# Optimization experiments

Hardware: AMD Instinct MI355X
Metric: run time of the kernel (lower is better)

## Reference

```python
import jax, jax.numpy as jnp
import numpy as np

N_COM = 100  # number of communities


def _gat(x, src, dst, ew, W, a_s, a_d):
    # Weighted multi-head GAT layer. x: [N,F], src/dst: [E], ew: [E]
    N = x.shape[0]
    H, dh = a_s.shape
    h = (x @ W).reshape(N, H, dh)              # [N,H,dh]
    hs, hd = h[src], h[dst]                     # [E,H,dh]
    e = jax.nn.leaky_relu((hs * a_s).sum(-1) + (hd * a_d).sum(-1), 0.2)  # [E,H]
    m = jax.ops.segment_max(e, dst, num_segments=N)  # [N,H] stable softmax max
    m = jnp.where(jnp.isfinite(m), m, 0.0)
    ex = jnp.exp(e - m[dst]) * ew[:, None]      # edge-weighted attention numerator
    den = jax.ops.segment_sum(ex, dst, num_segments=N)          # [N,H]
    num = jax.ops.segment_sum(ex[:, :, None] * hs, dst, num_segments=N)  # [N,H,dh]
    out = num / (den[:, :, None] + 1e-16)
    return jax.nn.elu(out.reshape(N, H * dh))


def _meso(x, part, D):
    # WeiPool_noW: degree-weighted mean pooling per community, scattered back to nodes
    num = jax.ops.segment_sum(D[:, None] * x, part, num_segments=N_COM)  # [C,d]
    den = jax.ops.segment_sum(D, part, num_segments=N_COM)               # [C]
    mean = num / (den[:, None] + 1e-16)
    return mean[part]                                                     # [N,d]


def _lstm_cell(h, c, x, Wx, Wh, b):
    z = x @ Wx + h @ Wh + b
    i, f, g, o = jnp.split(z, 4, axis=-1)
    c = jax.nn.sigmoid(f) * c + jax.nn.sigmoid(i) * jnp.tanh(g)
    h = jax.nn.sigmoid(o) * jnp.tanh(c)
    return h, c


def setup_inputs() -> dict:
    key = jax.random.key(0)
    ks = jax.random.split(key, 20)
    T, N, E, F = 8, 10000, 320000, 128
    H = 4
    d1, d2 = 128, 64            # micro_dims[1], micro_dims[2]
    d_rnn = 128                 # RNN_dims[1]; RNN input = 2*d2 = 128
    d_dec = 64                  # decoder_dims[1]
    s = 0.05
    inp = {
        'feat': jax.random.normal(ks[0], (T, N, F), jnp.float32),
        'edge_weight': jax.random.uniform(ks[1], (T, E), jnp.float32),
        'D': jax.random.uniform(ks[2], (T, N), jnp.float32),
        'W1': jax.random.normal(ks[3], (F, d1), jnp.float32) * s,
        'a_src1': jax.random.normal(ks[4], (H, d1 // H), jnp.float32) * s,
        'a_dst1': jax.random.normal(ks[5], (H, d1 // H), jnp.float32) * s,
        'W2': jax.random.normal(ks[6], (d1, d2), jnp.float32) * s,
        'a_src2': jax.random.normal(ks[7], (H, d2 // H), jnp.float32) * s,
        'a_dst2': jax.random.normal(ks[8], (H, d2 // H), jnp.float32) * s,
        'Wx': jax.random.normal(ks[9], (2 * d2, 4 * d_rnn), jnp.float32) * s,
        'Wh': jax.random.normal(ks[10], (d_rnn, 4 * d_rnn), jnp.float32) * s,
        'b_lstm': jnp.zeros((4 * d_rnn,), jnp.float32),
        'emb_W': jax.random.normal(ks[11], (d_rnn, d_dec), jnp.float32) * s,
        'emb_b': jnp.zeros((d_dec,), jnp.float32),
        'scal_W': jax.random.normal(ks[12], (d_rnn, d_dec), jnp.float32) * s,
        'scal_b': jnp.zeros((d_dec,), jnp.float32),
        'edge_index': jax.random.randint(ks[13], (T, 2, E), 0, N, jnp.int64),
        'partition': jax.random.randint(ks[14], (T, N), 0, N_COM, jnp.int64),
    }
    return inp


def reference(feat, edge_weight, D, W1, a_src1, a_dst1, W2, a_src2, a_dst2,
              Wx, Wh, b_lstm, emb_W, emb_b, scal_W, scal_b,
              edge_index, partition):
    T, N, _ = feat.shape
    src, dst = edge_index[:, 0], edge_index[:, 1]          # [T,E]
    gat = jax.vmap(_gat, in_axes=(0, 0, 0, 0, None, None, None))
    g1 = gat(feat, src, dst, edge_weight, W1, a_src1, a_dst1)   # [T,N,d1]
    g2 = gat(g1, src, dst, edge_weight, W2, a_src2, a_dst2)     # [T,N,d2]
    meso = jax.vmap(_meso)(g2, partition, D)                    # [T,N,d2]
    agg = jnp.concatenate([g2, meso], axis=-1)                  # [T,N,2*d2]

    d_h = Wh.shape[0]
    h0 = jnp.zeros((N, d_h), feat.dtype)

    def step(carry, x):
        h, c = carry
        h, c = _lstm_cell(h, c, x, Wx, Wh, b_lstm)
        return (h, c), h

    _, hs = jax.lax.scan(step, (h0, h0), agg)                   # [T,N,d_h]
    h_last = hs[-1]

    emb = jnp.tanh(h_last @ emb_W + emb_b)                      # decoder emb path
    emb = emb / jnp.linalg.norm(emb, axis=0, keepdims=True)     # F.normalize dim=0
    scal = jax.nn.sigmoid(h_last @ scal_W + scal_b)             # decoder scal path
    S = scal @ scal.T                                            # [N,N]
    G = emb @ emb.T
    sq = jnp.diag(G)
    dist = -(sq[:, None] + sq[None, :] - 2.0 * G)                # -||e_i - e_j||^2
    adj_est = 1.0 + jnp.tanh(dist * S)
    return adj_est
```

## Files before the change

### kernel.cpp

```cpp
#include <hip/hip_runtime.h>
#include <cstddef>
#include <cstdint>

#define T_   8
#define N_   10000
#define E_   320000
#define F_   128
#define D1_  128
#define D2_  64
#define DR_  128
#define NC_  100
#define TN_  (T_*N_)
#define TE_  (T_*E_)
#define NPAD_ 10112

typedef __attribute__((ext_vector_type(8))) short bf16x8;
typedef __attribute__((ext_vector_type(8))) ushort u16x8;
typedef __attribute__((ext_vector_type(4))) float f32x4;

__device__ __forceinline__ float bf2f(ushort u) {
    return __uint_as_float(((unsigned int)u) << 16);
}
__device__ __forceinline__ ushort f2bf(float f) {
    unsigned int u = __float_as_uint(f);
    unsigned int r = (u + 0x7FFFu + ((u >> 16) & 1u)) >> 16;
    return (ushort)r;
}
__device__ __forceinline__ float fast_tanh(float x) {
    float t = __expf(2.f * x);
    return 1.f - 2.f / (t + 1.f);
}
__device__ __forceinline__ float fast_sigmoid(float x) {
    return 1.f / (1.f + __expf(-x));
}

__global__ __launch_bounds__(256) void conv_feat(const float* __restrict__ src,
                                                 ushort* __restrict__ dst, int n8)
{
    int idx = blockIdx.x * 256 + threadIdx.x;
    if (idx >= n8) return;
    const float4* s = (const float4*)src + (size_t)idx * 2;
    float4 x = s[0], y = s[1];
    u16x8 o;
    o[0]=f2bf(x.x); o[1]=f2bf(x.y); o[2]=f2bf(x.z); o[3]=f2bf(x.w);
    o[4]=f2bf(y.x); o[5]=f2bf(y.y); o[6]=f2bf(y.z); o[7]=f2bf(y.w);
    *((u16x8*)dst + idx) = o;
}

__global__ __launch_bounds__(256) void conv_weights(
    const float* __restrict__ W1, const float* __restrict__ W2,
    const float* __restrict__ Wx, const float* __restrict__ Wh,
    const float* __restrict__ eW, const float* __restrict__ sW,
    ushort* __restrict__ W1T, ushort* __restrict__ W2T,
    ushort* __restrict__ WxT, ushort* __restrict__ WhT,
    ushort* __restrict__ eWT, ushort* __restrict__ sWT)
{
    int idx = blockIdx.x * 256 + threadIdx.x;
    if (idx < 16384)       { int n=idx>>7,   k=idx&127;            W1T[idx]=f2bf(W1[k*128+n]); }
    else if (idx < 24576)  { int l=idx-16384;  int n=l>>7,k=l&127; W2T[l]=f2bf(W2[k*64+n]); }
    else if (idx < 90112)  { int l=idx-24576;  int n=l>>7,k=l&127; WxT[l]=f2bf(Wx[k*512+n]); }
    else if (idx < 155648) { int l=idx-90112;  int n=l>>7,k=l&127; WhT[l]=f2bf(Wh[k*512+n]); }
    else if (idx < 163840) { int l=idx-155648; int n=l>>7,k=l&127; eWT[l]=f2bf(eW[k*64+n]); }
    else if (idx < 172032) { int l=idx-163840; int n=l>>7,k=l&127; sWT[l]=f2bf(sW[k*64+n]); }
}

__global__ __launch_bounds__(256) void gemm_bf16(
    const ushort* __restrict__ A, const ushort* __restrict__ BT,
    float* __restrict__ Cf, ushort* __restrict__ Cb,
    const float* __restrict__ bias, const float* __restrict__ addsrc,
    int M, int K, int Nc, int act)
{
    int w = threadIdx.x >> 6, lane = threadIdx.x & 63;
    int quad = lane >> 4, l16 = lane & 15;
    int m0 = blockIdx.y * 128 + w * 32;
    int n0 = blockIdx.x * 64;
    f32x4 zf = {0.f, 0.f, 0.f, 0.f};
    f32x4 acc[2][4];
    #pragma unroll
    for (int rt = 0; rt < 2; ++rt)
        #pragma unroll
        for (int ct = 0; ct < 4; ++ct) acc[rt][ct] = zf;

    for (int k0 = 0; k0 < K; k0 += 32) {
        int kk = k0 + quad * 8;
        bf16x8 a0 = *(const bf16x8*)(A + (size_t)(m0 + l16) * K + kk);
        bf16x8 a1 = *(const bf16x8*)(A + (size_t)(m0 + 16 + l16) * K + kk);
        bf16x8 b[4];
        #pragma unroll
        for (int ct = 0; ct < 4; ++ct)
            b[ct] = *(const bf16x8*)(BT + (size_t)(n0 + ct * 16 + l16) * K + kk);
        #pragma unroll
        for (int ct = 0; ct < 4; ++ct) {
            acc[0][ct] = __builtin_amdgcn_mfma_f32_16x16x32_bf16(a0, b[ct], acc[0][ct], 0, 0, 0);
            acc[1][ct] = __builtin_amdgcn_mfma_f32_16x16x32_bf16(a1, b[ct], acc[1][ct], 0, 0, 0);
        }
    }

    #pragma unroll
    for (int rt = 0; rt < 2; ++rt) {
        int ibase = m0 + rt * 16 + quad * 4;
        #pragma unroll
        for (int r = 0; r < 4; ++r) {
            int i = ibase + r;
            if (i >= M) continue;
            #pragma unroll
            for (int ct = 0; ct < 4; ++ct) {
                int j = n0 + ct * 16 + l16;
                float v = acc[rt][ct][r];
                if (bias)   v += bias[j];
                if (addsrc) v += addsrc[(size_t)i * Nc + j];
                if (act == 1)      v = fast_tanh(v);
                else if (act == 2) v = fast_sigmoid(v);
                if (Cf) Cf[(size_t)i * Nc + j] = v;
                if (Cb) Cb[(size_t)i * Nc + j] = f2bf(v);
            }
        }
    }
}

__global__ __launch_bounds__(256) void att_vec128(
    const ushort* __restrict__ h, const float* __restrict__ a_src,
    const float* __restrict__ a_dst, float* __restrict__ as_out,
    float* __restrict__ ad_out, int rows)
{
    int wid  = (blockIdx.x * 256 + threadIdx.x) >> 6;
    int lane = threadIdx.x & 63;
    if (wid >= rows) return;
    const ushort* hr = h + (size_t)wid * 128;
    float v0 = bf2f(hr[lane]), v1 = bf2f(hr[64 + lane]);
    float pa0 = v0 * a_src[lane], pa1 = v1 * a_src[64 + lane];
    float pd0 = v0 * a_dst[lane], pd1 = v1 * a_dst[64 + lane];
    #pragma unroll
    for (int m = 1; m <= 16; m <<= 1) {
        pa0 += __shfl_xor(pa0, m); pa1 += __shfl_xor(pa1, m);
        pd0 += __shfl_xor(pd0, m); pd1 += __shfl_xor(pd1, m);
    }
    if ((lane & 31) == 0) {
        int g = lane >> 5;
        as_out[wid * 4 + g] = pa0; as_out[wid * 4 + 2 + g] = pa1;
        ad_out[wid * 4 + g] = pd0; ad_out[wid * 4 + 2 + g] = pd1;
    }
}

__global__ __launch_bounds__(256) void att_vec64(
    const ushort* __restrict__ h, const float* __restrict__ a_src,
    const float* __restrict__ a_dst, float* __restrict__ as_out,
    float* __restrict__ ad_out, int rows)
{
    int wid  = (blockIdx.x * 256 + threadIdx.x) >> 6;
    int lane = threadIdx.x & 63;
    if (wid >= rows) return;
    float v = bf2f(h[(size_t)wid * 64 + lane]);
    float pa = v * a_src[lane], pd = v * a_dst[lane];
    #pragma unroll
    for (int m = 1; m <= 8; m <<= 1) { pa += __shfl_xor(pa, m); pd += __shfl_xor(pd, m); }
    if ((lane & 15) == 0) {
        int g = lane >> 4;
        as_out[wid * 4 + g] = pa; ad_out[wid * 4 + g] = pd;
    }
}

__global__ void count_edges(const int* __restrict__ eidx, int* __restrict__ counts)
{
    int idx = blockIdx.x * 256 + threadIdx.x;
    if (idx >= TE_) return;
    int t = idx / E_, e = idx - t * E_;
    int d = eidx[(size_t)t * 2 * E_ + E_ + e];
    atomicAdd(&counts[t * N_ + d], 1);
}

__global__ __launch_bounds__(1024) void scan_per_t(
    const int* __restrict__ counts, int* __restrict__ rowptr, int* __restrict__ cursor)
{
    const int CH = 10;
    int t = blockIdx.x, i = threadIdx.x;
    int base0 = t * N_;
    int cnt[CH];
    int s = 0;
    int g0 = i * CH;
    #pragma unroll
    for (int q = 0; q < CH; ++q) {
        int g = g0 + q;
        cnt[q] = (g < N_) ? counts[base0 + g] : 0;
        s += cnt[q];
    }
    __shared__ int buf[1024];
    buf[i] = s;
    __syncthreads();
    for (int off = 1; off < 1024; off <<= 1) {
        int v = (i >= off) ? buf[i - off] : 0;
        __syncthreads();
        buf[i] += v;
        __syncthreads();
    }
    int run = t * E_ + buf[i] - s;
    #pragma unroll
    for (int q = 0; q < CH; ++q) {
        int g = g0 + q;
        if (g < N_) {
            rowptr[base0 + g] = run;
            cursor[base0 + g] = run;
            run += cnt[q];
        }
    }
    if (t == T_ - 1 && i == 1023) rowptr[T_ * N_] = TE_;
}

__global__ void fill_csr(const int* __restrict__ eidx, const float* __restrict__ ew,
                         int* __restrict__ cursor, int* __restrict__ src_csr,
                         float* __restrict__ ew_csr)
{
    int idx = blockIdx.x * 256 + threadIdx.x;
    if (idx >= TE_) return;
    int t = idx / E_, e = idx - t * E_;
    int s = eidx[(size_t)t * 2 * E_ + e];
    int d = eidx[(size_t)t * 2 * E_ + E_ + e];
    float w = ew[(size_t)t * E_ + e];
    int pos = atomicAdd(&cursor[t * N_ + d], 1);
    src_csr[pos] = t * N_ + s;
    ew_csr[pos] = w;
}

__global__ __launch_bounds__(256) void gat_node_128(
    const ushort* __restrict__ h, const float* __restrict__ as,
    const float* __restrict__ ad, const int* __restrict__ rowptr,
    const int* __restrict__ src_csr, const float* __restrict__ ew_csr,
    ushort* __restrict__ outp, int rows)
{
    int wid  = (blockIdx.x * 256 + threadIdx.x) >> 6;
    int lane = threadIdx.x & 63;
    if (wid >= rows) return;
    int start = rowptr[wid], end = rowptr[wid + 1];
    int h0 = lane >> 5, h1 = 2 + h0;
    float ad0 = ad[wid * 4 + h0], ad1 = ad[wid * 4 + h1];
    float acc0 = 0.f, acc1 = 0.f, den0 = 0.f, den1 = 0.f;
    for (int p = start; p < end; ++p) {
        int s = src_csr[p];
        float w = ew_csr[p];
        float e0 = as[s * 4 + h0] + ad0; e0 = e0 > 0.f ? e0 : 0.2f * e0;
        float e1 = as[s * 4 + h1] + ad1; e1 = e1 > 0.f ? e1 : 0.2f * e1;
        float x0 = __expf(e0) * w;
        float x1 = __expf(e1) * w;
        den0 += x0; den1 += x1;
        const ushort* hs = h + (size_t)s * 128;
        acc0 += x0 * bf2f(hs[lane]);
        acc1 += x1 * bf2f(hs[64 + lane]);
    }
    float o0 = acc0 / (den0 + 1e-16f);
    float o1 = acc1 / (den1 + 1e-16f);
    o0 = o0 > 0.f ? o0 : (__expf(o0) - 1.f);
    o1 = o1 > 0.f ? o1 : (__expf(o1) - 1.f);
    outp[(size_t)wid * 128 + lane]      = f2bf(o0);
    outp[(size_t)wid * 128 + 64 + lane] = f2bf(o1);
}

__global__ __launch_bounds__(256) void gat_node_64(
    const ushort* __restrict__ h, const float* __restrict__ as,
    const float* __restrict__ ad, const int* __restrict__ rowptr,
    const int* __restrict__ src_csr, const float* __restrict__ ew_csr,
    ushort* __restrict__ outp, int rows)
{
    int wid  = (blockIdx.x * 256 + threadIdx.x) >> 6;
    int lane = threadIdx.x & 63;
    if (wid >= rows) return;
    int start = rowptr[wid], end = rowptr[wid + 1];
    int hh = lane >> 4;
    float adv = ad[wid * 4 + hh];
    float acc = 0.f, den = 0.f;
    for (int p = start; p < end; ++p) {
        int s = src_csr[p];
        float w = ew_csr[p];
        float e = as[s * 4 + hh] + adv; e = e > 0.f ? e : 0.2f * e;
        float x = __expf(e) * w;
        den += x;
        acc += x * bf2f(h[(size_t)s * 64 + lane]);
    }
    float o = acc / (den + 1e-16f);
    o = o > 0.f ? o : (__expf(o) - 1.f);
    outp[(size_t)wid * 64 + lane] = f2bf(o);
}

__global__ __launch_bounds__(256) void meso_acc(
    const ushort* __restrict__ g2, const int* __restrict__ part,
    const float* __restrict__ Dw, float* __restrict__ msum, float* __restrict__ mden)
{
    int wid  = (blockIdx.x * 256 + threadIdx.x) >> 6;
    int lane = threadIdx.x & 63;
    if (wid >= TN_) return;
    int t = wid / N_;
    int p = part[wid];
    float dv = Dw[wid];
    atomicAdd(&msum[((size_t)(t * NC_ + p) << 6) + lane], dv * bf2f(g2[(size_t)wid * 64 + lane]));
    if (lane == 0) atomicAdd(&mden[t * NC_ + p], dv);
}

__global__ void agg_assemble(
    const ushort* __restrict__ g2, const int* __restrict__ part,
    const float* __restrict__ msum, const float* __restrict__ mden,
    ushort* __restrict__ agg)
{
    int idx = blockIdx.x * 256 + threadIdx.x;
    int row = idx >> 7, d = idx & 127;
    ushort v;
    if (d < 64) {
        v = g2[(size_t)row * 64 + d];
    } else {
        int t = row / N_;
        int p = part[row];
        v = f2bf(msum[((size_t)(t * NC_ + p) << 6) + (d - 64)] / (mden[t * NC_ + p] + 1e-16f));
    }
    agg[idx] = v;
}

__global__ void lstm_cell(const float* __restrict__ z, float* __restrict__ c,
                          ushort* __restrict__ hb)
{
    int idx = blockIdx.x * 256 + threadIdx.x;
    int n = idx >> 7, j = idx & 127;
    const float* zr = z + (size_t)n * 512;
    float zi = zr[j], zf = zr[128 + j], zg = zr[256 + j], zo = zr[384 + j];
    float si = fast_sigmoid(zi);
    float sf = fast_sigmoid(zf);
    float so = fast_sigmoid(zo);
    float cn = sf * c[idx] + si * fast_tanh(zg);
    c[idx] = cn;
    hb[(size_t)n * 128 + j] = f2bf(so * fast_tanh(cn));
}

__global__ __launch_bounds__(256) void col_sumsq(const float* __restrict__ emb,
                                                 float* __restrict__ colss)
{
    int tid = threadIdx.x;
    int col = tid & 63, rq = tid >> 6;
    float s = 0.f;
    for (int r = blockIdx.x * 4 + rq; r < N_; r += 40 * 4) {
        float v = emb[(size_t)r * 64 + col];
        s += v * v;
    }
    __shared__ float red[256];
    red[tid] = s;
    __syncthreads();
    if (tid < 64)
        atomicAdd(&colss[tid], red[tid] + red[tid + 64] + red[tid + 128] + red[tid + 192]);
}

__global__ __launch_bounds__(256) void norm_rows(const float* __restrict__ emb,
                                                 const float* __restrict__ colss,
                                                 ushort* __restrict__ embb,
                                                 float* __restrict__ sq, int rows)
{
    int wid  = (blockIdx.x * 256 + threadIdx.x) >> 6;
    int lane = threadIdx.x & 63;
    if (wid >= rows) return;
    float nv = emb[(size_t)wid * 64 + lane] / sqrtf(colss[lane]);
    ushort ub = f2bf(nv);
    embb[(size_t)wid * 64 + lane] = ub;
    float nq = bf2f(ub);
    float q = nq * nq;
    #pragma unroll
    for (int m = 1; m <= 32; m <<= 1) q += __shfl_xor(q, m);
    if (lane == 0) sq[wid] = q;
}

#define FTJ_   5
#define FCOLS_ (FTJ_*128)

__global__ __launch_bounds__(256) void final_adj_mfma(
    const ushort* __restrict__ embb, const ushort* __restrict__ scalb,
    const float* __restrict__ sq, float* __restrict__ outp)
{
    __shared__ float cur[128][132];
    __shared__ float edg[2][64][16];

    int w = threadIdx.x >> 6, lane = threadIdx.x & 63;
    int quad = lane >> 4, l16 = lane & 15;
    int bi = blockIdx.y * 128;
    int Wb = blockIdx.x * FCOLS_;
    int wi = bi + (w >> 1) * 64;

    float sqi[4];
    #pragma unroll
    for (int rt = 0; rt < 4; ++rt) sqi[rt] = sq[wi + rt * 16 + l16];

    int tLast = (N_ - 1 - Wb) / 128;
    if (tLast > FTJ_ - 1) tLast = FTJ_ - 1;

    for (int t = 0; t <= tLast; ++t) {
        int Wt = Wb + t * 128;
        int wj = Wt + (w & 1) * 64;

        f32x4 zf = {0.f, 0.f, 0.f, 0.f};
        f32x4 accG[4][4], accS[4][4];
        #pragma unroll
        for (int rt = 0; rt < 4; ++rt)
            #pragma unroll
            for (int ct = 0; ct < 4; ++ct) { accG[rt][ct] = zf; accS[rt][ct] = zf; }

        #pragma unroll
        for (int ks = 0; ks < 2; ++ks) {
            int k0 = ks * 32 + quad * 8;
            bf16x8 ae[4], af[4], be[4], bs[4];
            #pragma unroll
            for (int q = 0; q < 4; ++q) {
                int ri = wi + q * 16 + l16;
                int rj = wj + q * 16 + l16;
                ae[q] = *(const bf16x8*)(embb  + (size_t)ri * 64 + k0);
                af[q] = *(const bf16x8*)(scalb + (size_t)ri * 64 + k0);
                be[q] = *(const bf16x8*)(embb  + (size_t)rj * 64 + k0);
                bs[q] = *(const bf16x8*)(scalb + (size_t)rj * 64 + k0);
            }
            #pragma unroll
            for (int rt = 0; rt < 4; ++rt)
                #pragma unroll
                for (int ct = 0; ct < 4; ++ct) {
                    accG[rt][ct] = __builtin_amdgcn_mfma_f32_16x16x32_bf16(be[ct], ae[rt], accG[rt][ct], 0, 0, 0);
                    accS[rt][ct] = __builtin_amdgcn_mfma_f32_16x16x32_bf16(bs[ct], af[rt], accS[rt][ct], 0, 0, 0);
                }
        }

        __syncthreads();

        #pragma unroll
        for (int rt = 0; rt < 4; ++rt) {
            int li = (w >> 1) * 64 + rt * 16 + l16;
            float si = sqi[rt];
            #pragma unroll
            for (int ct = 0; ct < 4; ++ct) {
                int lj = (w & 1) * 64 + ct * 16 + quad * 4;
                const float4 sj = *(const float4*)(sq + Wt + lj);
                float sjr[4] = { sj.x, sj.y, sj.z, sj.w };
                f32x4 v;
                #pragma unroll
                for (int r = 0; r < 4; ++r) {
                    float G = accG[rt][ct][r], S = accS[rt][ct][r];
                    float dist = 2.f * G - si - sjr[r];
                    float e = __expf(2.f * dist * S);
                    v[r] = 2.f - 2.f / (e + 1.f);
                }
                *(f32x4*)&cur[li][lj] = v;
                if ((w & 1) && ct == 3 && (li & 1))
                    *(f32x4*)&edg[t & 1][li >> 1][quad * 4] = v;
            }
        }

        __syncthreads();

        int lane5 = lane & 31;
        #pragma unroll
        for (int pass = 0; pass < 16; ++pass) {
            int r = pass * 8 + (lane >> 5) * 4 + w;
            int i = bi + r;
            if (i < N_) {
                if (!(r & 1)) {
                    int gcol = Wt + lane5 * 4;
                    if (gcol < N_)
                        __builtin_nontemporal_store(*(const f32x4*)&cur[r][lane5 * 4],
                            (f32x4*)(outp + (size_t)i * N_ + gcol));
                } else {
                    int gcol = Wt - 16 + lane5 * 4;
                    if ((t > 0 || lane5 >= 4) && gcol >= 0 && gcol < N_) {
                        f32x4 v;
                        if (lane5 < 4) v = *(const f32x4*)&edg[(t & 1) ^ 1][r >> 1][lane5 * 4];
                        else           v = *(const f32x4*)&cur[r][lane5 * 4 - 16];
                        __builtin_nontemporal_store(v,
                            (f32x4*)(outp + (size_t)i * N_ + gcol));
                    }
                }
            }
        }
    }

    {
        int tid = threadIdx.x;
        int r = ((tid >> 2) << 1) | 1;
        int k = (tid & 3) * 4;
        int i = bi + r;
        int gcol = Wb + tLast * 128 + 112 + k;
        if (i < N_ && gcol < N_) {
            f32x4 v = *(const f32x4*)&cur[r][112 + k];
            __builtin_nontemporal_store(v, (f32x4*)(outp + (size_t)i * N_ + gcol));
        }
    }
}

extern "C" void kernel_launch(void* const* d_in, const int* in_sizes, int n_in,
                              void* d_out, int out_size, void* d_ws, size_t ws_size,
                              hipStream_t stream)
{
    (void)in_sizes; (void)n_in; (void)out_size; (void)ws_size;
    const float* feat    = (const float*)d_in[0];
    const float* eweight = (const float*)d_in[1];
    const float* Dw      = (const float*)d_in[2];
    const float* W1      = (const float*)d_in[3];
    const float* a_src1  = (const float*)d_in[4];
    const float* a_dst1  = (const float*)d_in[5];
    const float* W2      = (const float*)d_in[6];
    const float* a_src2  = (const float*)d_in[7];
    const float* a_dst2  = (const float*)d_in[8];
    const float* Wx      = (const float*)d_in[9];
    const float* Wh      = (const float*)d_in[10];
    const float* b_lstm  = (const float*)d_in[11];
    const float* emb_W   = (const float*)d_in[12];
    const float* emb_b   = (const float*)d_in[13];
    const float* scal_W  = (const float*)d_in[14];
    const float* scal_b  = (const float*)d_in[15];
    const int*   eidx    = (const int*)d_in[16];
    const int*   part    = (const int*)d_in[17];

    float* out = (float*)d_out;
    ushort* h1b   = (ushort*)(out + 0);
    ushort* g1b   = (ushort*)(out + 5120000);
    ushort* h2b   = (ushort*)(out + 10240000);
    ushort* g2b   = (ushort*)(out + 12800000);
    float* as1    = out + 15360000;
    float* ad1    = out + 15680000;
    float* as2    = out + 16000000;
    float* ad2    = out + 16320000;
    int*   rowptr = (int*)(out + 16640000);
    int*   cursor = (int*)(out + 16720064);
    int*   counts = (int*)(out + 16800064);
    int*   src_csr= (int*)(out + 16880064);
    float* ew_csr = out + 19440064;
    float* msum   = out + 22000064;
    float* mden   = out + 22051264;
    ushort* aggb  = (ushort*)(out + 22052064);
    float* ZX     = out + 27172064;
    float* zbuf   = out + 68132064;
    float* cstate = out + 73252064;
    ushort* hbf   = (ushort*)(out + 74532064);
    ushort* featb = (ushort*)(out + 75179232);
    ushort* W1T   = (ushort*)(out + 80299232);
    ushort* W2T   = (ushort*)(out + 80307424);
    ushort* WxT   = (ushort*)(out + 80311520);
    ushort* WhT   = (ushort*)(out + 80344288);
    ushort* eWT   = (ushort*)(out + 80377056);
    ushort* sWT   = (ushort*)(out + 80381152);
    float* embf   = out + 80385248;
    float* colss  = out + 81025248;

    ushort* embb  = (ushort*)d_ws;
    ushort* scalb = embb + (size_t)NPAD_ * 64;
    float*  sq    = (float*)(scalb + (size_t)NPAD_ * 64);

    hipMemsetAsync(counts, 0, TN_ * sizeof(int), stream);
    hipMemsetAsync(msum, 0, (T_ * NC_ * 64 + T_ * NC_) * sizeof(float), stream);
    hipMemsetAsync(cstate, 0, (size_t)N_ * DR_ * sizeof(float), stream);
    hipMemsetAsync(hbf, 0, (size_t)NPAD_ * DR_ * sizeof(ushort), stream);
    hipMemsetAsync(colss, 0, 64 * sizeof(float), stream);

    conv_feat<<<5000, 256, 0, stream>>>(feat, featb, TN_ * F_ / 8);
    conv_weights<<<672, 256, 0, stream>>>(W1, W2, Wx, Wh, emb_W, scal_W,
                                          W1T, W2T, WxT, WhT, eWT, sWT);

    gemm_bf16<<<dim3(2, 625), 256, 0, stream>>>(featb, W1T, nullptr, h1b, nullptr, nullptr, TN_, 128, 128, 0);
    att_vec128<<<TN_/4, 256, 0, stream>>>(h1b, a_src1, a_dst1, as1, ad1, TN_);
    count_edges<<<(TE_+255)/256, 256, 0, stream>>>(eidx, counts);
    scan_per_t<<<T_, 1024, 0, stream>>>(counts, rowptr, cursor);
    fill_csr<<<(TE_+255)/256, 256, 0, stream>>>(eidx, eweight, cursor, src_csr, ew_csr);
    gat_node_128<<<TN_/4, 256, 0, stream>>>(h1b, as1, ad1, rowptr, src_csr, ew_csr, g1b, TN_);

    gemm_bf16<<<dim3(1, 625), 256, 0, stream>>>(g1b, W2T, nullptr, h2b, nullptr, nullptr, TN_, 128, 64, 0);
    att_vec64<<<TN_/4, 256, 0, stream>>>(h2b, a_src2, a_dst2, as2, ad2, TN_);
    gat_node_64<<<TN_/4, 256, 0, stream>>>(h2b, as2, ad2, rowptr, src_csr, ew_csr, g2b, TN_);

    meso_acc<<<TN_/4, 256, 0, stream>>>(g2b, part, Dw, msum, mden);
    agg_assemble<<<TN_*128/256, 256, 0, stream>>>(g2b, part, msum, mden, aggb);

    gemm_bf16<<<dim3(8, 625), 256, 0, stream>>>(aggb, WxT, ZX, nullptr, b_lstm, nullptr, TN_, 128, 512, 0);
    for (int t = 0; t < T_; ++t) {
        gemm_bf16<<<dim3(8, 79), 256, 0, stream>>>(hbf, WhT, zbuf, nullptr, nullptr,
                                                   ZX + (size_t)t * N_ * 512, N_, 128, 512, 0);
        lstm_cell<<<N_*DR_/256, 256, 0, stream>>>(zbuf, cstate, hbf);
    }

    gemm_bf16<<<dim3(1, 79), 256, 0, stream>>>(hbf, eWT, embf, nullptr, emb_b, nullptr, N_, 128, 64, 1);
    gemm_bf16<<<dim3(1, 79), 256, 0, stream>>>(hbf, sWT, nullptr, scalb, scal_b, nullptr, N_, 128, 64, 2);
    col_sumsq<<<40, 256, 0, stream>>>(embf, colss);
    norm_rows<<<(N_+3)/4, 256, 0, stream>>>(embf, colss, embb, sq, N_);

    final_adj_mfma<<<dim3(16, 79), 256, 0, stream>>>(embb, scalb, sq, out);
}
```

Baseline: 1.870 ms.

## Fuse LSTM recurrent GEMM with cell update and unroll GAT edge loops

Replaces the per-timestep recurrent gemm plus separate lstm_cell kernel with one MFMA kernel. It computes h@Wh for a 32-row tile, adds the precomputed input projection, stages the gates in shared memory and applies the cell update in place. This removes the fp32 zbuf write and read-back and one launch per step. Separately, both GAT aggregation kernels now process four edges per iteration and load the four per-head attention scores with a single float4. This exposes more independent gathers. Costs are a large shared-memory tile and higher register pressure.

```diff
diff --git a/kernel.cpp b/kernel.cpp
--- a/kernel.cpp
+++ b/kernel.cpp
@@ -231,21 +231,46 @@
     int lane = threadIdx.x & 63;
     if (wid >= rows) return;
     int start = rowptr[wid], end = rowptr[wid + 1];
-    int h0 = lane >> 5, h1 = 2 + h0;
-    float ad0 = ad[wid * 4 + h0], ad1 = ad[wid * 4 + h1];
+    int h0 = lane >> 5;
+    float ad0 = ad[wid * 4 + h0], ad1 = ad[wid * 4 + 2 + h0];
     float acc0 = 0.f, acc1 = 0.f, den0 = 0.f, den1 = 0.f;
-    for (int p = start; p < end; ++p) {
+
+    int p = start;
+    for (; p + 4 <= end; p += 4) {
+        int s0 = src_csr[p+0], s1 = src_csr[p+1], s2 = src_csr[p+2], s3 = src_csr[p+3];
+        float w0 = ew_csr[p+0], w1 = ew_csr[p+1], w2 = ew_csr[p+2], w3 = ew_csr[p+3];
+        float4 A0 = *(const float4*)(as + (size_t)s0 * 4);
+        float4 A1 = *(const float4*)(as + (size_t)s1 * 4);
+        float4 A2 = *(const float4*)(as + (size_t)s2 * 4);
+        float4 A3 = *(const float4*)(as + (size_t)s3 * 4);
+        const ushort* q0 = h + (size_t)s0 * 128;
+        const ushort* q1 = h + (size_t)s1 * 128;
+        const ushort* q2 = h + (size_t)s2 * 128;
+        const ushort* q3 = h + (size_t)s3 * 128;
+        float hx0 = bf2f(q0[lane]), hy0 = bf2f(q0[64 + lane]);
+        float hx1 = bf2f(q1[lane]), hy1 = bf2f(q1[64 + lane]);
+        float hx2 = bf2f(q2[lane]), hy2 = bf2f(q2[64 + lane]);
+        float hx3 = bf2f(q3[lane]), hy3 = bf2f(q3[64 + lane]);
+        #define GSTEP(AA, ww, hx, hy) { \
+            float e0 = (h0 ? AA.y : AA.x) + ad0; e0 = e0 > 0.f ? e0 : 0.2f * e0; \
+            float e1 = (h0 ? AA.w : AA.z) + ad1; e1 = e1 > 0.f ? e1 : 0.2f * e1; \
+            float x0 = __expf(e0) * ww, x1 = __expf(e1) * ww; \
+            den0 += x0; den1 += x1; acc0 += x0 * hx; acc1 += x1 * hy; }
+        GSTEP(A0, w0, hx0, hy0)
+        GSTEP(A1, w1, hx1, hy1)
+        GSTEP(A2, w2, hx2, hy2)
+        GSTEP(A3, w3, hx3, hy3)
+    }
+    for (; p < end; ++p) {
         int s = src_csr[p];
         float w = ew_csr[p];
-        float e0 = as[s * 4 + h0] + ad0; e0 = e0 > 0.f ? e0 : 0.2f * e0;
-        float e1 = as[s * 4 + h1] + ad1; e1 = e1 > 0.f ? e1 : 0.2f * e1;
-        float x0 = __expf(e0) * w;
-        float x1 = __expf(e1) * w;
-        den0 += x0; den1 += x1;
-        const ushort* hs = h + (size_t)s * 128;
-        acc0 += x0 * bf2f(hs[lane]);
-        acc1 += x1 * bf2f(hs[64 + lane]);
-    }
+        float4 A = *(const float4*)(as + (size_t)s * 4);
+        const ushort* q = h + (size_t)s * 128;
+        float hx = bf2f(q[lane]), hy = bf2f(q[64 + lane]);
+        GSTEP(A, w, hx, hy)
+    }
+    #undef GSTEP
+
     float o0 = acc0 / (den0 + 1e-16f);
     float o1 = acc1 / (den1 + 1e-16f);
     o0 = o0 > 0.f ? o0 : (__expf(o0) - 1.f);
@@ -267,14 +292,38 @@
     int hh = lane >> 4;
     float adv = ad[wid * 4 + hh];
     float acc = 0.f, den = 0.f;
-    for (int p = start; p < end; ++p) {
+
+    int p = start;
+    for (; p + 4 <= end; p += 4) {
+        int s0 = src_csr[p+0], s1 = src_csr[p+1], s2 = src_csr[p+2], s3 = src_csr[p+3];
+        float w0 = ew_csr[p+0], w1 = ew_csr[p+1], w2 = ew_csr[p+2], w3 = ew_csr[p+3];
+        float4 A0 = *(const float4*)(as + (size_t)s0 * 4);
+        float4 A1 = *(const float4*)(as + (size_t)s1 * 4);
+        float4 A2 = *(const float4*)(as + (size_t)s2 * 4);
+        float4 A3 = *(const float4*)(as + (size_t)s3 * 4);
+        float hv0 = bf2f(h[(size_t)s0 * 64 + lane]);
+        float hv1 = bf2f(h[(size_t)s1 * 64 + lane]);
+        float hv2 = bf2f(h[(size_t)s2 * 64 + lane]);
+        float hv3 = bf2f(h[(size_t)s3 * 64 + lane]);
+        #define GSTEP64(AA, ww, hv) { \
+            float e = (hh & 2 ? (hh & 1 ? AA.w : AA.z) : (hh & 1 ? AA.y : AA.x)) + adv; \
+            e = e > 0.f ? e : 0.2f * e; \
+            float x = __expf(e) * ww; \
+            den += x; acc += x * hv; }
+        GSTEP64(A0, w0, hv0)
+        GSTEP64(A1, w1, hv1)
+        GSTEP64(A2, w2, hv2)
+        GSTEP64(A3, w3, hv3)
+    }
+    for (; p < end; ++p) {
         int s = src_csr[p];
         float w = ew_csr[p];
-        float e = as[s * 4 + hh] + adv; e = e > 0.f ? e : 0.2f * e;
-        float x = __expf(e) * w;
-        den += x;
-        acc += x * bf2f(h[(size_t)s * 64 + lane]);
-    }
+        float4 A = *(const float4*)(as + (size_t)s * 4);
+        float hv = bf2f(h[(size_t)s * 64 + lane]);
+        GSTEP64(A, w, hv)
+    }
+    #undef GSTEP64
+
     float o = acc / (den + 1e-16f);
     o = o > 0.f ? o : (__expf(o) - 1.f);
     outp[(size_t)wid * 64 + lane] = f2bf(o);
@@ -312,19 +361,84 @@
     agg[idx] = v;
 }
 
-__global__ void lstm_cell(const float* __restrict__ z, float* __restrict__ c,
-                          ushort* __restrict__ hb)
-{
-    int idx = blockIdx.x * 256 + threadIdx.x;
-    int n = idx >> 7, j = idx & 127;
-    const float* zr = z + (size_t)n * 512;
-    float zi = zr[j], zf = zr[128 + j], zg = zr[256 + j], zo = zr[384 + j];
-    float si = fast_sigmoid(zi);
-    float sf = fast_sigmoid(zf);
-    float so = fast_sigmoid(zo);
-    float cn = sf * c[idx] + si * fast_tanh(zg);
-    c[idx] = cn;
-    hb[(size_t)n * 128 + j] = f2bf(so * fast_tanh(cn));
+__global__ __launch_bounds__(512) void lstm_fused(
+    const ushort* __restrict__ hin, const ushort* __restrict__ WhT,
+    const float* __restrict__ zx, float* __restrict__ c,
+    ushort* __restrict__ hout)
+{
+    __shared__ float zt[32][516];
+    int w = threadIdx.x >> 6, lane = threadIdx.x & 63;
+    int quad = lane >> 4, l16 = lane & 15;
+    int m0 = blockIdx.x * 32;
+    int n0 = w * 64;
+
+    f32x4 zf = {0.f, 0.f, 0.f, 0.f};
+    f32x4 acc[2][4];
+    #pragma unroll
+    for (int rt = 0; rt < 2; ++rt)
+        #pragma unroll
+        for (int ct = 0; ct < 4; ++ct) acc[rt][ct] = zf;
+
+    #pragma unroll
+    for (int k0 = 0; k0 < 128; k0 += 32) {
+        int kk = k0 + quad * 8;
+        bf16x8 a0 = *(const bf16x8*)(hin + (size_t)(m0 + l16) * 128 + kk);
+        bf16x8 a1 = *(const bf16x8*)(hin + (size_t)(m0 + 16 + l16) * 128 + kk);
+        bf16x8 b[4];
+        #pragma unroll
+        for (int ct = 0; ct < 4; ++ct)
+            b[ct] = *(const bf16x8*)(WhT + (size_t)(n0 + ct * 16 + l16) * 128 + kk);
+        #pragma unroll
+        for (int ct = 0; ct < 4; ++ct) {
+            acc[0][ct] = __builtin_amdgcn_mfma_f32_16x16x32_bf16(a0, b[ct], acc[0][ct], 0, 0, 0);
+            acc[1][ct] = __builtin_amdgcn_mfma_f32_16x16x32_bf16(a1, b[ct], acc[1][ct], 0, 0, 0);
+        }
+    }
+
+    #pragma unroll
+    for (int rt = 0; rt < 2; ++rt) {
+        #pragma unroll
+        for (int r = 0; r < 4; ++r) {
+            int li = rt * 16 + quad * 4 + r;
+            size_t gi = (size_t)(m0 + li);
+            #pragma unroll
+            for (int ct = 0; ct < 4; ++ct) {
+                int j = n0 + ct * 16 + l16;
+                zt[li][j] = acc[rt][ct][r] + zx[gi * 512 + j];
+            }
+        }
+    }
+    __syncthreads();
+
+    int r  = threadIdx.x >> 4;
+    int j0 = (threadIdx.x & 15) * 8;
+    int gi = m0 + r;
+    if (gi < N_) {
+        f32x4 vi[2], vf[2], vg[2], vo[2], vc[2];
+        #pragma unroll
+        for (int hb = 0; hb < 2; ++hb) {
+            int jj = j0 + hb * 4;
+            vi[hb] = *(const f32x4*)&zt[r][jj];
+            vf[hb] = *(const f32x4*)&zt[r][128 + jj];
+            vg[hb] = *(const f32x4*)&zt[r][256 + jj];
+            vo[hb] = *(const f32x4*)&zt[r][384 + jj];
+            vc[hb] = *(const f32x4*)(c + (size_t)gi * 128 + jj);
+        }
+        u16x8 ho;
+        #pragma unroll
+        for (int e = 0; e < 8; ++e) {
+            int hb = e >> 2, q = e & 3;
+            float si = fast_sigmoid(vi[hb][q]);
+            float sf = fast_sigmoid(vf[hb][q]);
+            float so = fast_sigmoid(vo[hb][q]);
+            float cn = sf * vc[hb][q] + si * fast_tanh(vg[hb][q]);
+            vc[hb][q] = cn;
+            ho[e] = f2bf(so * fast_tanh(cn));
+        }
+        *(f32x4*)(c + (size_t)gi * 128 + j0)     = vc[0];
+        *(f32x4*)(c + (size_t)gi * 128 + j0 + 4) = vc[1];
+        *(u16x8*)(hout + (size_t)gi * 128 + j0)  = ho;
+    }
 }
 
 __global__ __launch_bounds__(256) void col_sumsq(const float* __restrict__ emb,
@@ -525,7 +639,6 @@
     float* mden   = out + 22051264;
     ushort* aggb  = (ushort*)(out + 22052064);
     float* ZX     = out + 27172064;
-    float* zbuf   = out + 68132064;
     float* cstate = out + 73252064;
     ushort* hbf   = (ushort*)(out + 74532064);
     ushort* featb = (ushort*)(out + 75179232);
@@ -567,11 +680,9 @@
     agg_assemble<<<TN_*128/256, 256, 0, stream>>>(g2b, part, msum, mden, aggb);
 
     gemm_bf16<<<dim3(8, 625), 256, 0, stream>>>(aggb, WxT, ZX, nullptr, b_lstm, nullptr, TN_, 128, 512, 0);
-    for (int t = 0; t < T_; ++t) {
-        gemm_bf16<<<dim3(8, 79), 256, 0, stream>>>(hbf, WhT, zbuf, nullptr, nullptr,
-                                                   ZX + (size_t)t * N_ * 512, N_, 128, 512, 0);
-        lstm_cell<<<N_*DR_/256, 256, 0, stream>>>(zbuf, cstate, hbf);
-    }
+    for (int t = 0; t < T_; ++t)
+        lstm_fused<<<(N_ + 31) / 32, 512, 0, stream>>>(hbf, WhT, ZX + (size_t)t * N_ * 512,
+                                                       cstate, hbf);
 
     gemm_bf16<<<dim3(1, 79), 256, 0, stream>>>(hbf, eWT, embf, nullptr, emb_b, nullptr, N_, 128, 64, 1);
     gemm_bf16<<<dim3(1, 79), 256, 0, stream>>>(hbf, sWT, nullptr, scalb, scal_b, nullptr, N_, 128, 64, 2);
```

Result: faster. 1.640 ms (-12.3%).
